# Optimization experiments

Hardware: AMD Instinct MI355X
Metric: run time of the kernel (lower is better)

The kernel has to match this reference:

```python
import jax, jax.numpy as jnp
import numpy as np

T, N, XD, H, Z, E = 6, 4096, 64, 256, 128, 131072


def setup_inputs() -> dict:
    key = jax.random.key(0)
    ks = jax.random.split(key, 16)
    f32 = jnp.float32
    def rn(k, shp):
        return jax.random.normal(k, shp, f32)
    def gl(k, shp):  # glorot-ish init, scaled by fan_in
        return jax.random.normal(k, shp, f32) * np.float32(1.0 / np.sqrt(shp[-2]))
    return {
        "x": rn(ks[0], (T, N, XD)),
        "edges": jax.random.randint(ks[1], (T, 2, E), 0, N, dtype=jnp.int32),
        "eps": rn(ks[2], (T, N, Z)),
        "drop_u": jax.random.uniform(ks[3], (T, N, Z), f32),
        "phi_x_w": gl(ks[4], (XD, H)), "phi_x_b": jnp.zeros((H,), f32),
        "phi_z_w": gl(ks[5], (Z, H)), "phi_z_b": jnp.zeros((H,), f32),
        "enc_w": gl(ks[6], (2 * H, H)),
        "enc_mu_w": gl(ks[7], (H, Z)),
        "enc_lv_w": gl(ks[8], (H, Z)),
        "prior_w": gl(ks[9], (H, H)), "prior_b": jnp.zeros((H,), f32),
        "prior_mu_w": gl(ks[10], (H, Z)), "prior_mu_b": jnp.zeros((Z,), f32),
        "prior_lv_w": gl(ks[11], (H, Z)), "prior_lv_b": jnp.zeros((Z,), f32),
        "gru_wx": gl(ks[12], (4, 2 * H, H)),  # gates i,f,o,c; x-side GCN weights
        "gru_wh": gl(ks[13], (4, H, H)),      # gates i,f,o,c; h-side GCN weights
    }


def reference(x, edges, eps, drop_u, phi_x_w, phi_x_b, phi_z_w, phi_z_b,
              enc_w, enc_mu_w, enc_lv_w, prior_w, prior_b,
              prior_mu_w, prior_mu_b, prior_lv_w, prior_lv_b,
              gru_wx, gru_wh):
    T_, N_, _ = x.shape
    H_ = phi_x_w.shape[1]
    h = jnp.zeros((N_, H_), x.dtype)
    c = jnp.zeros((N_, H_), x.dtype)
    loop = jnp.arange(N_, dtype=edges.dtype)
    enc_mus, prior_mus = [], []
    dec_t = None
    for t in range(T_):  # fixed small T; edge structure differs per step
        row = jnp.concatenate([edges[t, 0], loop])  # add self loops
        col = jnp.concatenate([edges[t, 1], loop])
        deg = jax.ops.segment_sum(jnp.ones(row.shape, x.dtype), row, num_segments=N_)
        dinv = jnp.where(deg > 0, jax.lax.rsqrt(deg), jnp.zeros((), x.dtype))
        norm = (dinv[row] * dinv[col])[:, None]

        def gcn(xx, W):
            # GCNConv: xW, gather at col, scale by sym-norm, scatter-add at row
            return jax.ops.segment_sum(norm * (xx @ W)[col], row, num_segments=N_)

        phi_x_t = jax.nn.relu(x[t] @ phi_x_w + phi_x_b)
        enc_t = jax.nn.relu(gcn(jnp.concatenate([phi_x_t, h], axis=1), enc_w))
        enc_mu_t = gcn(enc_t, enc_mu_w)
        enc_std_t = jax.nn.softplus(gcn(enc_t, enc_lv_w))
        prior_t = jax.nn.relu(h @ prior_w + prior_b)
        prior_mu_t = prior_t @ prior_mu_w + prior_mu_b
        _prior_std_t = jax.nn.softplus(prior_t @ prior_lv_w + prior_lv_b)  # computed as in original, unused in returns
        z_t = eps[t] * enc_std_t + enc_mu_t  # original: eps.mul(logvar).add_(mu)
        phi_z_t = jax.nn.relu(z_t @ phi_z_w + phi_z_b)
        # InnerProductDecoder with dropout(p=0.5, training=True), identity act
        z_drop = jnp.where(drop_u[t] < 0.5, z_t * 2.0, jnp.zeros((), x.dtype))
        dec_t = z_drop @ z_drop.T  # [N, N]
        # graph-LSTM step (n_layer = 1)
        xin = jnp.concatenate([phi_x_t, phi_z_t], axis=1)  # [N, 2H]
        gi = jax.nn.sigmoid(gcn(xin, gru_wx[0]) + gcn(h, gru_wh[0]))
        gf = jax.nn.sigmoid(gcn(xin, gru_wx[1]) + gcn(h, gru_wh[1]))
        go = jax.nn.sigmoid(gcn(xin, gru_wx[2]) + gcn(h, gru_wh[2]))
        ct = jnp.tanh(gcn(xin, gru_wx[3]) + gcn(h, gru_wh[3]))
        c_new = gf * h + gi * ct    # faithful to original: F_g * h[i] (not c)
        h_new = go * jnp.tanh(c)    # faithful to original: uses old c[i]
        h, c = h_new, c_new
        enc_mus.append(enc_mu_t)
        prior_mus.append(prior_mu_t)
    return jnp.stack(enc_mus), jnp.stack(prior_mus), h[None], dec_t
```

## Files before the change

### kernel.cpp

```cpp
#include <hip/hip_runtime.h>
#include <hip/hip_bf16.h>
#include <math.h>

#define T_  6
#define NN  4096
#define XD_ 64
#define H_  256
#define ZZ  128
#define EE  131072

typedef unsigned short u16;
typedef __attribute__((ext_vector_type(8))) short short8;
typedef __attribute__((ext_vector_type(4))) float f32x4;

__device__ __forceinline__ float bf2f(u16 u) { return __uint_as_float(((unsigned)u) << 16); }
__device__ __forceinline__ u16 f2bf(float f) {
    unsigned x = __float_as_uint(f);
    return (u16)((x + 0x7FFFu + ((x >> 16) & 1u)) >> 16);
}

__global__ void k_deg(const int* __restrict__ edges, int* __restrict__ degcnt) {
    int t = blockIdx.y;
    int e = blockIdx.x * 256 + threadIdx.x;
    const int* rows = edges + (size_t)t * 2 * EE;
    atomicAdd(&degcnt[t * NN + rows[e]], 1);
}

__global__ void k_scan_dinv(const int* __restrict__ degcnt_all,
                            int* __restrict__ row_start_all,
                            int* __restrict__ cursor_all,
                            float* __restrict__ dinv_all) {
    __shared__ int sbuf[1024];
    int tt = blockIdx.x;
    const int* degcnt = degcnt_all + tt * NN;
    int* row_start = row_start_all + tt * (NN + 1);
    int* cursor = cursor_all + tt * NN;
    float* dinv = dinv_all + tt * NN;
    int t = threadIdx.x;
    int b = t * 4;
    int v0 = degcnt[b + 0], v1 = degcnt[b + 1], v2 = degcnt[b + 2], v3 = degcnt[b + 3];
    dinv[b + 0] = rsqrtf((float)(v0 + 1));
    dinv[b + 1] = rsqrtf((float)(v1 + 1));
    dinv[b + 2] = rsqrtf((float)(v2 + 1));
    dinv[b + 3] = rsqrtf((float)(v3 + 1));
    int s = v0 + v1 + v2 + v3;
    sbuf[t] = s;
    __syncthreads();
    for (int off = 1; off < 1024; off <<= 1) {
        int x = sbuf[t];
        int y = (t >= off) ? sbuf[t - off] : 0;
        __syncthreads();
        sbuf[t] = x + y;
        __syncthreads();
    }
    int excl = sbuf[t] - s;
    int r0 = excl, r1 = excl + v0, r2 = r1 + v1, r3 = r2 + v2;
    row_start[b + 0] = r0; cursor[b + 0] = r0;
    row_start[b + 1] = r1; cursor[b + 1] = r1;
    row_start[b + 2] = r2; cursor[b + 2] = r2;
    row_start[b + 3] = r3; cursor[b + 3] = r3;
    if (t == 1023) row_start[NN] = r3 + v3;
}

__global__ void k_scatter(const int* __restrict__ edges,
                          int* __restrict__ cursor, const float* __restrict__ dinv,
                          int* __restrict__ col_idx, float* __restrict__ val) {
    int t = blockIdx.y;
    int e = blockIdx.x * 256 + threadIdx.x;
    const int* rows = edges + (size_t)t * 2 * EE;
    const int* cols = rows + EE;
    int r = rows[e], cc = cols[e];
    int pos = atomicAdd(&cursor[t * NN + r], 1);
    col_idx[(size_t)t * EE + pos] = cc;
    val[(size_t)t * EE + pos] = dinv[t * NN + r] * dinv[t * NN + cc];
}

__device__ __forceinline__ void sp_row(const u16* __restrict__ Y,
                                       const int* __restrict__ row_start,
                                       const int* __restrict__ col_idx,
                                       const float* __restrict__ val,
                                       const float* __restrict__ dinv,
                                       u16* __restrict__ outp, int ldo,
                                       int r, float (*red)[64][4]) {
    int lane = threadIdx.x & 63, w = threadIdx.x >> 6;
    int s0 = row_start[r], s1 = row_start[r + 1];
    int deg = s1 - s0;
    int e0 = s0 + ((deg * w) >> 2);
    int e1 = s0 + ((deg * (w + 1)) >> 2);
    float a1[4] = {0.f, 0.f, 0.f, 0.f};
    for (int base = e0; base < e1; base += 64) {
        int n = e1 - base; if (n > 64) n = 64;
        int cl = 0; float vl = 0.f;
        if (base + lane < e1) { cl = col_idx[base + lane]; vl = val[base + lane]; }
        for (int e = 0; e < n; ++e) {
            int cc = __shfl(cl, e);
            float v = __shfl(vl, e);
            ushort4 y = *(const ushort4*)(Y + (size_t)cc * H_ + lane * 4);
            a1[0] += v * bf2f(y.x); a1[1] += v * bf2f(y.y);
            a1[2] += v * bf2f(y.z); a1[3] += v * bf2f(y.w);
        }
    }
#pragma unroll
    for (int j = 0; j < 4; ++j) red[w][lane][j] = a1[j];
    __syncthreads();
    if (w == 0) {
        float dr = dinv[r], sc = dr * dr;
#pragma unroll
        for (int j = 0; j < 4; ++j)
#pragma unroll
            for (int ww = 1; ww < 4; ++ww) a1[j] += red[ww][lane][j];
        ushort4 ys = *(const ushort4*)(Y + (size_t)r * H_ + lane * 4);
        a1[0] += sc * bf2f(ys.x); a1[1] += sc * bf2f(ys.y);
        a1[2] += sc * bf2f(ys.z); a1[3] += sc * bf2f(ys.w);
        *(ushort4*)(outp + (size_t)r * ldo + lane * 4) =
            make_ushort4(f2bf(a1[0]), f2bf(a1[1]), f2bf(a1[2]), f2bf(a1[3]));
    }
}

__global__ void k_spmm(const u16* __restrict__ Y1,
                       const int* __restrict__ row_start_all, const int* __restrict__ col_idx_all,
                       const float* __restrict__ val_all, const float* __restrict__ dinv_all,
                       u16* __restrict__ out1, int ldo,
                       long long sY, long long sO) {
    __shared__ float red[4][64][4];
    int t = blockIdx.y;
    sp_row(Y1 + (size_t)t * sY, row_start_all + (size_t)t * (NN + 1),
           col_idx_all + (size_t)t * EE, val_all + (size_t)t * EE,
           dinv_all + (size_t)t * NN, out1 + (size_t)t * sO, ldo,
           blockIdx.x, red);
}

template<int MF>
__device__ __forceinline__ void mm_core(const u16* __restrict__ A, int lda,
                                        const u16* __restrict__ BT, int ldbt, int K,
                                        int row0, int col0,
                                        f32x4 acc[MF][MF], char* smem) {
    constexpr int TILE = MF * 32;
    u16* As = (u16*)smem;
    u16* Bs = As + TILE * 64;
    const int lane = threadIdx.x & 63;
    const int w = threadIdx.x >> 6;
    const int wr = (w >> 1) * (TILE / 2);
    const int wc = (w & 1) * (TILE / 2);

    int gRow[MF], gCol[MF];
#pragma unroll
    for (int i = 0; i < MF; ++i) {
        int G = (w * MF + i) * 64 + lane;
        int r = G >> 3;
        gRow[i] = r;
        gCol[i] = ((G & 7) ^ (r & 7)) << 3;
    }

    for (int k0 = 0; k0 < K; k0 += 64) {
#pragma unroll
        for (int i = 0; i < MF; ++i) {
            const u16* sa = A + (size_t)(row0 + gRow[i]) * lda + k0 + gCol[i];
            __builtin_amdgcn_global_load_lds(
                (const __attribute__((address_space(1))) void*)sa,
                (__attribute__((address_space(3))) void*)(As + (w * MF + i) * 512), 16, 0, 0);
            const u16* sb = BT + (size_t)(col0 + gRow[i]) * ldbt + k0 + gCol[i];
            __builtin_amdgcn_global_load_lds(
                (const __attribute__((address_space(1))) void*)sb,
                (__attribute__((address_space(3))) void*)(Bs + (w * MF + i) * 512), 16, 0, 0);
        }
        __syncthreads();
#pragma unroll
        for (int kk = 0; kk < 2; ++kk) {
            short8 a[MF], b[MF];
#pragma unroll
            for (int mf = 0; mf < MF; ++mf) {
                int r = wr + mf * 16 + (lane & 15);
                int off = (r * 128 + kk * 64 + (lane >> 4) * 16) ^ ((r & 7) << 4);
                a[mf] = *(const short8*)((const char*)As + off);
            }
#pragma unroll
            for (int nf = 0; nf < MF; ++nf) {
                int r = wc + nf * 16 + (lane & 15);
                int off = (r * 128 + kk * 64 + (lane >> 4) * 16) ^ ((r & 7) << 4);
                b[nf] = *(const short8*)((const char*)Bs + off);
            }
#pragma unroll
            for (int mf = 0; mf < MF; ++mf)
#pragma unroll
                for (int nf = 0; nf < MF; ++nf)
                    acc[mf][nf] = __builtin_amdgcn_mfma_f32_16x16x32_bf16(
                        a[mf], b[nf], acc[mf][nf], 0, 0, 0);
        }
        __syncthreads();
    }
}

template<int MF>
__launch_bounds__(256)
__global__ void k_mm(const u16* __restrict__ A, int lda,
                     const u16* __restrict__ BT, int ldbt, int K,
                     float* __restrict__ C0, int ldc0,
                     u16* __restrict__ C1, int ldc1,
                     const float* __restrict__ bias, int act,
                     float* __restrict__ C2,
                     const float* __restrict__ du, u16* __restrict__ zdOut) {
    constexpr int TILE = MF * 32;
    constexpr int STAGE_B = TILE * 64 * 2 * 2;
    constexpr int EPI_B = (MF == 2) ? 64 * 68 * 4 : 0;
    constexpr int SMEM_B = STAGE_B > EPI_B ? STAGE_B : EPI_B;
    __shared__ alignas(16) char smem[SMEM_B];

    const int tid = threadIdx.x;
    const int lane = tid & 63;
    const int w = tid >> 6;
    const int row0 = blockIdx.y * TILE;
    const int col0 = blockIdx.x * TILE;
    const int wr = (w >> 1) * (TILE / 2);
    const int wc = (w & 1) * (TILE / 2);

    f32x4 acc[MF][MF];
#pragma unroll
    for (int i = 0; i < MF; ++i)
#pragma unroll
        for (int j = 0; j < MF; ++j)
            acc[i][j] = f32x4{0.f, 0.f, 0.f, 0.f};

    mm_core<MF>(A, lda, BT, ldbt, K, row0, col0, acc, smem);

    const int ci = lane & 15;
    const int ri = (lane >> 4) * 4;

    if constexpr (MF == 2) {
        if (act == 4) {
            float (*epi)[68] = (float(*)[68])smem;
#pragma unroll
            for (int mf = 0; mf < 2; ++mf)
#pragma unroll
                for (int nf = 0; nf < 2; ++nf)
#pragma unroll
                    for (int i = 0; i < 4; ++i)
                        epi[wr + mf * 16 + ri + i][wc + nf * 16 + ci] = acc[mf][nf][i];
            __syncthreads();
            float* muo = C0; const float* eps = C2; u16* zo = C1;
#pragma unroll
            for (int k = 0; k < 8; ++k) {
                int p = tid + k * 256;
                int row = p >> 5, jl = p & 31;
                float mu = epi[row][jl * 2];
                float sp = epi[row][jl * 2 + 1];
                float sd = (sp > 20.f) ? sp : log1pf(expf(sp));
                int idx = (row0 + row) * ZZ + (col0 >> 1) + jl;
                muo[idx] = mu;
                u16 z16 = f2bf(eps[idx] * sd + mu);
                zo[idx] = z16;
                if (zdOut)
                    zdOut[idx] = (du[idx] < 0.5f) ? f2bf(2.f * bf2f(z16)) : (u16)0;
            }
            return;
        }
    }

#pragma unroll
    for (int mf = 0; mf < MF; ++mf) {
#pragma unroll
        for (int nf = 0; nf < MF; ++nf) {
            int row = row0 + wr + mf * 16 + ri;
            int col = col0 + wc + nf * 16 + ci;
            if (C1) {
                float bv = bias ? bias[col] : 0.f;
#pragma unroll
                for (int i = 0; i < 4; ++i) {
                    float v = acc[mf][nf][i] + bv;
                    if (act == 1) v = fmaxf(v, 0.f);
                    C1[(size_t)(row + i) * ldc1 + col] = f2bf(v);
                }
            } else {
                float bv = bias ? bias[col] : 0.f;
#pragma unroll
                for (int i = 0; i < 4; ++i)
                    C0[(size_t)(row + i) * ldc0 + col] = acc[mf][nf][i] + bv;
            }
        }
    }
}

__launch_bounds__(256)
__global__ void k_dual(const u16* __restrict__ A0, int lda0, const u16* __restrict__ BT0,
                       int ldbt0, int K0, u16* __restrict__ C0d, int ldc0d,
                       const float* __restrict__ b0,
                       const u16* __restrict__ A1, int lda1, const u16* __restrict__ BT1,
                       int ldbt1, int K1, u16* __restrict__ C1d, int ldc1d,
                       const float* __restrict__ b1) {
    __shared__ alignas(16) char smem[16384];
    const int z = blockIdx.z;
    const u16* A = z ? A1 : A0;   int lda = z ? lda1 : lda0;
    const u16* BT = z ? BT1 : BT0; int ldbt = z ? ldbt1 : ldbt0;
    int K = z ? K1 : K0;
    u16* C = z ? C1d : C0d;       int ldc = z ? ldc1d : ldc0d;
    const float* bias = z ? b1 : b0;

    const int lane = threadIdx.x & 63;
    const int w = threadIdx.x >> 6;
    const int row0 = blockIdx.y * 64;
    const int col0 = blockIdx.x * 64;
    const int wr = (w >> 1) * 32, wc = (w & 1) * 32;

    f32x4 acc[2][2];
#pragma unroll
    for (int i = 0; i < 2; ++i)
#pragma unroll
        for (int j = 0; j < 2; ++j) acc[i][j] = f32x4{0.f, 0.f, 0.f, 0.f};
    mm_core<2>(A, lda, BT, ldbt, K, row0, col0, acc, smem);

    const int ci = lane & 15, ri = (lane >> 4) * 4;
#pragma unroll
    for (int mf = 0; mf < 2; ++mf)
#pragma unroll
        for (int nf = 0; nf < 2; ++nf) {
            int row = row0 + wr + mf * 16 + ri;
            int col = col0 + wc + nf * 16 + ci;
            float bv = bias ? bias[col] : 0.f;
#pragma unroll
            for (int i = 0; i < 4; ++i)
                C[(size_t)(row + i) * ldc + col] = f2bf(fmaxf(acc[mf][nf][i] + bv, 0.f));
        }
}

__launch_bounds__(256)
__global__ void k_sp_mm(const u16* __restrict__ Y, const int* __restrict__ row_start,
                        const int* __restrict__ col_idx, const float* __restrict__ val,
                        const float* __restrict__ dinv, u16* __restrict__ spOut,
                        const u16* __restrict__ A, int lda, const u16* __restrict__ BT,
                        int ldbt, int K, float* __restrict__ C0, int ldc0,
                        const float* __restrict__ bias) {
    __shared__ alignas(16) char smem[16384];
    int bid = blockIdx.x;
    if (bid < NN) {
        sp_row(Y, row_start, col_idx, val, dinv, spOut, H_, bid, (float(*)[64][4])smem);
        return;
    }
    int b2 = bid - NN;
    const int row0 = (b2 >> 1) * 64;
    const int col0 = (b2 & 1) * 64;
    const int lane = threadIdx.x & 63;
    const int w = threadIdx.x >> 6;
    const int wr = (w >> 1) * 32, wc = (w & 1) * 32;
    f32x4 acc[2][2];
#pragma unroll
    for (int i = 0; i < 2; ++i)
#pragma unroll
        for (int j = 0; j < 2; ++j) acc[i][j] = f32x4{0.f, 0.f, 0.f, 0.f};
    mm_core<2>(A, lda, BT, ldbt, K, row0, col0, acc, smem);
    const int ci = lane & 15, ri = (lane >> 4) * 4;
#pragma unroll
    for (int mf = 0; mf < 2; ++mf)
#pragma unroll
        for (int nf = 0; nf < 2; ++nf) {
            int row = row0 + wr + mf * 16 + ri;
            int col = col0 + wc + nf * 16 + ci;
            float bv = bias[col];
#pragma unroll
            for (int i = 0; i < 4; ++i)
                C0[(size_t)(row + i) * ldc0 + col] = acc[mf][nf][i] + bv;
        }
}

__launch_bounds__(256)
__global__ void k_gates(const u16* __restrict__ XIN, const u16* __restrict__ BgT,
                        float* __restrict__ h, float* __restrict__ c,
                        u16* __restrict__ hbf, float* __restrict__ hOut,
                        int skipSH) {
    __shared__ alignas(16) char smem[64 * 68 * 4];
    u16* As = (u16*)smem;
    u16* Bs = As + 64 * 64;
    const int tid = threadIdx.x;
    const int lane = tid & 63;
    const int w = tid >> 6;
    const int row0 = blockIdx.y * 64;
    const int col0 = blockIdx.x * 64;
    const int wr = (w >> 1) * 32;
    const int wc = (w & 1) * 32;

    f32x4 acc[2][2];
#pragma unroll
    for (int i = 0; i < 2; ++i)
#pragma unroll
        for (int j = 0; j < 2; ++j) acc[i][j] = f32x4{0.f, 0.f, 0.f, 0.f};

    int gRow[2], gCol[2];
#pragma unroll
    for (int i = 0; i < 2; ++i) {
        int G = (w * 2 + i) * 64 + lane;
        int r = G >> 3;
        gRow[i] = r;
        gCol[i] = ((G & 7) ^ (r & 7)) << 3;
    }

    const int nIter = skipSH ? 8 : 12;
    for (int it = 0; it < nIter; ++it) {
        int k0 = it * 64 + ((skipSH && it >= 4) ? 256 : 0);
#pragma unroll
        for (int i = 0; i < 2; ++i) {
            const u16* sa = XIN + (size_t)(row0 + gRow[i]) * 768 + k0 + gCol[i];
            __builtin_amdgcn_global_load_lds(
                (const __attribute__((address_space(1))) void*)sa,
                (__attribute__((address_space(3))) void*)(As + (w * 2 + i) * 512), 16, 0, 0);
            const u16* sb = BgT + (size_t)(col0 + gRow[i]) * 768 + k0 + gCol[i];
            __builtin_amdgcn_global_load_lds(
                (const __attribute__((address_space(1))) void*)sb,
                (__attribute__((address_space(3))) void*)(Bs + (w * 2 + i) * 512), 16, 0, 0);
        }
        __syncthreads();
#pragma unroll
        for (int kk = 0; kk < 2; ++kk) {
            short8 a[2], b[2];
#pragma unroll
            for (int mf = 0; mf < 2; ++mf) {
                int r = wr + mf * 16 + (lane & 15);
                int off = (r * 128 + kk * 64 + (lane >> 4) * 16) ^ ((r & 7) << 4);
                a[mf] = *(const short8*)((const char*)As + off);
            }
#pragma unroll
            for (int nf = 0; nf < 2; ++nf) {
                int r = wc + nf * 16 + (lane & 15);
                int off = (r * 128 + kk * 64 + (lane >> 4) * 16) ^ ((r & 7) << 4);
                b[nf] = *(const short8*)((const char*)Bs + off);
            }
#pragma unroll
            for (int mf = 0; mf < 2; ++mf)
#pragma unroll
                for (int nf = 0; nf < 2; ++nf)
                    acc[mf][nf] = __builtin_amdgcn_mfma_f32_16x16x32_bf16(
                        a[mf], b[nf], acc[mf][nf], 0, 0, 0);
        }
        __syncthreads();
    }

    const int ci = lane & 15;
    const int ri = (lane >> 4) * 4;
    float (*epi)[68] = (float(*)[68])smem;
#pragma unroll
    for (int mf = 0; mf < 2; ++mf)
#pragma unroll
        for (int nf = 0; nf < 2; ++nf)
#pragma unroll
            for (int i = 0; i < 4; ++i)
                epi[wr + mf * 16 + ri + i][wc + nf * 16 + ci] = acc[mf][nf][i];
    __syncthreads();
#pragma unroll
    for (int k = 0; k < 4; ++k) {
        int p = tid + k * 256;
        int row = p >> 4, jl = p & 15;
        float4 g4 = *(const float4*)&epi[row][jl * 4];
        float gi = 1.f / (1.f + expf(-g4.x));
        float gf = 1.f / (1.f + expf(-g4.y));
        float go = 1.f / (1.f + expf(-g4.z));
        float ct = tanhf(g4.w);
        int idx = (row0 + row) * H_ + (col0 >> 2) + jl;
        float ho = h[idx], co = c[idx];
        float cn = gf * ho + gi * ct;
        float hn = go * tanhf(co);
        h[idx] = hn;
        c[idx] = cn;
        hbf[idx] = f2bf(hn);
        if (hOut) hOut[idx] = hn;
    }
}

__global__ void k_cvt(const float* __restrict__ in, u16* __restrict__ outp, int n4) {
    int i = blockIdx.x * 256 + threadIdx.x;
    if (i >= n4) return;
    float4 v = ((const float4*)in)[i];
    ((ushort4*)outp)[i] = make_ushort4(f2bf(v.x), f2bf(v.y), f2bf(v.z), f2bf(v.w));
}

__global__ void k_prep(const float* __restrict__ phi_x_w, const float* __restrict__ phi_z_w,
                       const float* __restrict__ enc_w, const float* __restrict__ prior_w,
                       const float* __restrict__ prior_mu_w,
                       const float* __restrict__ enc_mu_w, const float* __restrict__ enc_lv_w,
                       const float* __restrict__ gru_wx, const float* __restrict__ gru_wh,
                       u16* __restrict__ phi_x_wT, u16* __restrict__ phi_z_wT,
                       u16* __restrict__ enc_wT, u16* __restrict__ prior_wT,
                       u16* __restrict__ prior_mu_wT, u16* __restrict__ mulvT,
                       u16* __restrict__ BgT) {
    int idx = blockIdx.x * 256 + threadIdx.x;
    if (idx < 16384) {
        int j = idx >> 6, k = idx & 63;
        phi_x_wT[idx] = f2bf(phi_x_w[k * 256 + j]);
        return;
    }
    idx -= 16384;
    if (idx < 32768) {
        int j = idx >> 7, k = idx & 127;
        phi_z_wT[idx] = f2bf(phi_z_w[k * 256 + j]);
        return;
    }
    idx -= 32768;
    if (idx < 131072) {
        int j = idx >> 9, k = idx & 511;
        enc_wT[idx] = f2bf(enc_w[k * 256 + j]);
        return;
    }
    idx -= 131072;
    if (idx < 65536) {
        int j = idx >> 8, k = idx & 255;
        prior_wT[idx] = f2bf(prior_w[k * 256 + j]);
        return;
    }
    idx -= 65536;
    if (idx < 32768) {
        int j = idx >> 8, k = idx & 255;
        prior_mu_wT[idx] = f2bf(prior_mu_w[k * 128 + j]);
        return;
    }
    idx -= 32768;
    if (idx < 65536) {
        int cp = idx >> 8, k = idx & 255;
        int j = cp >> 1, s = cp & 1;
        float v = s ? enc_lv_w[k * 128 + j] : enc_mu_w[k * 128 + j];
        mulvT[idx] = f2bf(v);
        return;
    }
    idx -= 65536;
    if (idx < 786432) {
        int cp = idx / 768, k = idx % 768;
        int g = cp & 3, j = cp >> 2;
        float v;
        if (k < 256)      v = gru_wx[((size_t)g * 512 + k) * 256 + j];
        else if (k < 512) v = gru_wh[((size_t)g * 256 + (k - 256)) * 256 + j];
        else              v = gru_wx[((size_t)g * 512 + (k - 256)) * 256 + j];
        BgT[idx] = f2bf(v);
    }
}

extern "C" void kernel_launch(void* const* d_in, const int* in_sizes, int n_in,
                              void* d_out_v, int out_size, void* d_ws, size_t ws_size,
                              hipStream_t stream) {
    (void)in_sizes; (void)n_in; (void)out_size;
    const float* x          = (const float*)d_in[0];
    const int*   edges      = (const int*)d_in[1];
    const float* eps        = (const float*)d_in[2];
    const float* drop_u     = (const float*)d_in[3];
    const float* phi_x_w    = (const float*)d_in[4];
    const float* phi_x_b    = (const float*)d_in[5];
    const float* phi_z_w    = (const float*)d_in[6];
    const float* phi_z_b    = (const float*)d_in[7];
    const float* enc_w      = (const float*)d_in[8];
    const float* enc_mu_w   = (const float*)d_in[9];
    const float* enc_lv_w   = (const float*)d_in[10];
    const float* prior_w    = (const float*)d_in[11];
    const float* prior_b    = (const float*)d_in[12];
    const float* prior_mu_w = (const float*)d_in[13];
    const float* prior_mu_b = (const float*)d_in[14];
    const float* gru_wx     = (const float*)d_in[17];
    const float* gru_wh     = (const float*)d_in[18];
    float* out = (float*)d_out_v;

    char* base = (char*)d_ws;
    size_t cur = 0;
    auto carve = [&](size_t bytes) -> void* {
        void* p = base + cur;
        cur += (bytes + 255) & ~(size_t)255;
        return p;
    };
    float* h         = (float*)carve((size_t)NN * H_ * 4);
    float* c         = (float*)carve((size_t)NN * H_ * 4);
    u16* h_bf        = (u16*)carve((size_t)NN * H_ * 2);
    size_t hcz_bytes = cur;
    float* dinv      = (float*)carve((size_t)T_ * NN * 4);
    int*   degcnt    = (int*)carve((size_t)T_ * NN * 4);
    int*   row_start = (int*)carve((size_t)T_ * (NN + 1) * 4);
    int*   cursor    = (int*)carve((size_t)T_ * NN * 4);
    int*   col_idx   = (int*)carve((size_t)T_ * EE * 4);
    float* val       = (float*)carve((size_t)T_ * EE * 4);
    u16* x_bf        = (u16*)carve((size_t)T_ * NN * XD_ * 2);
    u16* phi6        = (u16*)carve((size_t)T_ * NN * H_ * 2);
    u16* phi         = (u16*)carve((size_t)NN * H_ * 2);
    u16* enc_t       = (u16*)carve((size_t)NN * H_ * 2);
    u16* SEb         = (u16*)carve((size_t)NN * H_ * 2);
    u16* prior_t     = (u16*)carve((size_t)NN * H_ * 2);
    u16* XIN6        = (u16*)carve((size_t)T_ * NN * 768 * 2);
    u16* zbuf        = (u16*)carve((size_t)NN * ZZ * 2);
    u16* zd          = (u16*)carve((size_t)NN * ZZ * 2);
    u16* phi_x_wT    = (u16*)carve((size_t)XD_ * H_ * 2);
    u16* phi_z_wT    = (u16*)carve((size_t)ZZ * H_ * 2);
    u16* enc_wT      = (u16*)carve((size_t)512 * H_ * 2);
    u16* prior_wT    = (u16*)carve((size_t)H_ * H_ * 2);
    u16* prior_mu_wT = (u16*)carve((size_t)ZZ * H_ * 2);
    u16* mulvT       = (u16*)carve((size_t)H_ * H_ * 2);
    u16* BgT         = (u16*)carve((size_t)1024 * 768 * 2);
    if (cur > ws_size) return;

    const size_t NZ = (size_t)NN * ZZ;
    const size_t HOFF = (size_t)2 * T_ * NZ;
    const size_t DECOFF = HOFF + (size_t)NN * H_;

    k_cvt<<<(T_ * NN * XD_ / 4 + 255) / 256, 256, 0, stream>>>(x, x_bf, T_ * NN * XD_ / 4);
    k_prep<<<(1130496 + 255) / 256, 256, 0, stream>>>(
        phi_x_w, phi_z_w, enc_w, prior_w, prior_mu_w, enc_mu_w, enc_lv_w,
        gru_wx, gru_wh,
        phi_x_wT, phi_z_wT, enc_wT, prior_wT, prior_mu_wT, mulvT, BgT);

    hipMemsetAsync(degcnt, 0, (size_t)T_ * NN * 4, stream);
    k_deg<<<dim3(EE / 256, T_), 256, 0, stream>>>(edges, degcnt);
    k_scan_dinv<<<T_, 1024, 0, stream>>>(degcnt, row_start, cursor, dinv);
    k_scatter<<<dim3(EE / 256, T_), 256, 0, stream>>>(edges, cursor, dinv, col_idx, val);

    k_mm<2><<<dim3(4, (T_ * NN) / 64), 256, 0, stream>>>(x_bf, XD_, phi_x_wT, XD_, XD_,
        nullptr, 0, phi6, H_, phi_x_b, 1, nullptr, nullptr, nullptr);
    k_spmm<<<dim3(NN, T_), 256, 0, stream>>>(phi6, row_start, col_idx, val, dinv,
        XIN6, 768, (long long)NN * H_, (long long)NN * 768);

    hipMemsetAsync(h, 0, hcz_bytes, stream);

    for (int t = 0; t < T_; ++t) {
        const int* rs_t = row_start + (size_t)t * (NN + 1);
        const int* ci_t = col_idx + (size_t)t * EE;
        const float* vv_t = val + (size_t)t * EE;
        const float* dv_t = dinv + (size_t)t * NN;
        u16* xin_t = XIN6 + (size_t)t * NN * 768;
        int last = (t == T_ - 1);

        if (t > 0)
            k_spmm<<<dim3(NN, 1), 256, 0, stream>>>(h_bf, rs_t, ci_t, vv_t, dv_t,
                                                    xin_t + 256, 768, 0, 0);
        k_dual<<<dim3(4, 64, 2), 256, 0, stream>>>(
            xin_t, 768, enc_wT, 512, (t == 0) ? 256 : 512, enc_t, H_, nullptr,
            h_bf, H_, prior_wT, H_, H_, prior_t, H_, prior_b);
        k_sp_mm<<<NN + 128, 256, 0, stream>>>(enc_t, rs_t, ci_t, vv_t, dv_t, SEb,
            prior_t, H_, prior_mu_wT, H_, H_,
            out + (size_t)(T_ + t) * NZ, ZZ, prior_mu_b);
        k_mm<2><<<dim3(4, 64), 256, 0, stream>>>(SEb, H_, mulvT, H_, H_,
            out + (size_t)t * NZ, 0, zbuf, 0, nullptr, 4, (float*)(eps + (size_t)t * NZ),
            last ? drop_u + (size_t)t * NZ : nullptr, last ? zd : nullptr);
        k_mm<2><<<dim3(4, 64), 256, 0, stream>>>(zbuf, ZZ, phi_z_wT, ZZ, ZZ,
            nullptr, 0, phi, H_, phi_z_b, 1, nullptr, nullptr, nullptr);
        k_spmm<<<dim3(NN, 1), 256, 0, stream>>>(phi, rs_t, ci_t, vv_t, dv_t,
                                                xin_t + 512, 768, 0, 0);
        k_gates<<<dim3(16, 64), 256, 0, stream>>>(xin_t, BgT, h, c, h_bf,
            last ? out + HOFF : nullptr, t == 0);
    }

    k_mm<4><<<dim3(32, 32), 256, 0, stream>>>(zd, ZZ, zd, ZZ, ZZ,
        out + DECOFF, NN, nullptr, 0, nullptr, 0, nullptr, nullptr, nullptr);
}
```

Baseline: 613.6 us.

## Use one wave per SpMM row, regroup kernel fusions, enlarge gate tile

The sparse row aggregation now gives each wavefront a whole row, with two edges in flight per iteration and 16-byte loads. This removes the LDS reduction and __syncthreads across four waves, and each block now covers four rows. The per-step kernel pairing is reshuffled: the h-side SpMM is fused with the prior matmul, and the prior-mu matmul is fused into k_dual, whose z-slice skips its unused column blocks. The enc SpMM becomes a standalone launch. k_gates uses 128-row tiles, so fewer blocks each reuse the weight tile across more rows, at the cost of more registers and LDS per block.

```diff
diff --git a/kernel.cpp b/kernel.cpp
--- a/kernel.cpp
+++ b/kernel.cpp
@@ -11,6 +11,7 @@
 
 typedef unsigned short u16;
 typedef __attribute__((ext_vector_type(8))) short short8;
+typedef __attribute__((ext_vector_type(8))) unsigned short u16x8;
 typedef __attribute__((ext_vector_type(4))) float f32x4;
 
 __device__ __forceinline__ float bf2f(u16 u) { return __uint_as_float(((unsigned)u) << 16); }
@@ -75,45 +76,39 @@
     val[(size_t)t * EE + pos] = dinv[t * NN + r] * dinv[t * NN + cc];
 }
 
-__device__ __forceinline__ void sp_row(const u16* __restrict__ Y,
-                                       const int* __restrict__ row_start,
-                                       const int* __restrict__ col_idx,
-                                       const float* __restrict__ val,
-                                       const float* __restrict__ dinv,
-                                       u16* __restrict__ outp, int ldo,
-                                       int r, float (*red)[64][4]) {
-    int lane = threadIdx.x & 63, w = threadIdx.x >> 6;
+__device__ __forceinline__ void sp_row_wave(const u16* __restrict__ Y,
+                                            const int* __restrict__ row_start,
+                                            const int* __restrict__ col_idx,
+                                            const float* __restrict__ val,
+                                            const float* __restrict__ dinv,
+                                            u16* __restrict__ outp, int ldo, int r) {
+    int lane = threadIdx.x & 63;
+    int half = lane >> 5;
+    int cg = lane & 31;
     int s0 = row_start[r], s1 = row_start[r + 1];
-    int deg = s1 - s0;
-    int e0 = s0 + ((deg * w) >> 2);
-    int e1 = s0 + ((deg * (w + 1)) >> 2);
-    float a1[4] = {0.f, 0.f, 0.f, 0.f};
-    for (int base = e0; base < e1; base += 64) {
-        int n = e1 - base; if (n > 64) n = 64;
+    float a[8] = {0.f, 0.f, 0.f, 0.f, 0.f, 0.f, 0.f, 0.f};
+    for (int base = s0; base < s1; base += 64) {
+        int n = s1 - base; if (n > 64) n = 64;
         int cl = 0; float vl = 0.f;
-        if (base + lane < e1) { cl = col_idx[base + lane]; vl = val[base + lane]; }
-        for (int e = 0; e < n; ++e) {
-            int cc = __shfl(cl, e);
-            float v = __shfl(vl, e);
-            ushort4 y = *(const ushort4*)(Y + (size_t)cc * H_ + lane * 4);
-            a1[0] += v * bf2f(y.x); a1[1] += v * bf2f(y.y);
-            a1[2] += v * bf2f(y.z); a1[3] += v * bf2f(y.w);
-        }
-    }
-#pragma unroll
-    for (int j = 0; j < 4; ++j) red[w][lane][j] = a1[j];
-    __syncthreads();
-    if (w == 0) {
+        if (base + lane < s1) { cl = col_idx[base + lane]; vl = val[base + lane]; }
+        for (int e = 0; e < n; e += 2) {
+            int ei = e + half;
+            int cc = __shfl(cl, ei);
+            float v = (ei < n) ? __shfl(vl, ei) : 0.f;
+            u16x8 y = *(const u16x8*)(Y + (size_t)cc * H_ + cg * 8);
+#pragma unroll
+            for (int j = 0; j < 8; ++j) a[j] += v * bf2f(y[j]);
+        }
+    }
+#pragma unroll
+    for (int j = 0; j < 8; ++j) a[j] += __shfl_xor(a[j], 32);
+    if (half == 0) {
         float dr = dinv[r], sc = dr * dr;
-#pragma unroll
-        for (int j = 0; j < 4; ++j)
-#pragma unroll
-            for (int ww = 1; ww < 4; ++ww) a1[j] += red[ww][lane][j];
-        ushort4 ys = *(const ushort4*)(Y + (size_t)r * H_ + lane * 4);
-        a1[0] += sc * bf2f(ys.x); a1[1] += sc * bf2f(ys.y);
-        a1[2] += sc * bf2f(ys.z); a1[3] += sc * bf2f(ys.w);
-        *(ushort4*)(outp + (size_t)r * ldo + lane * 4) =
-            make_ushort4(f2bf(a1[0]), f2bf(a1[1]), f2bf(a1[2]), f2bf(a1[3]));
+        u16x8 ys = *(const u16x8*)(Y + (size_t)r * H_ + cg * 8);
+        u16x8 o;
+#pragma unroll
+        for (int j = 0; j < 8; ++j) o[j] = f2bf(a[j] + sc * bf2f(ys[j]));
+        *(u16x8*)(outp + (size_t)r * ldo + cg * 8) = o;
     }
 }
 
@@ -122,12 +117,12 @@
                        const float* __restrict__ val_all, const float* __restrict__ dinv_all,
                        u16* __restrict__ out1, int ldo,
                        long long sY, long long sO) {
-    __shared__ float red[4][64][4];
     int t = blockIdx.y;
-    sp_row(Y1 + (size_t)t * sY, row_start_all + (size_t)t * (NN + 1),
-           col_idx_all + (size_t)t * EE, val_all + (size_t)t * EE,
-           dinv_all + (size_t)t * NN, out1 + (size_t)t * sO, ldo,
-           blockIdx.x, red);
+    int w = threadIdx.x >> 6;
+    sp_row_wave(Y1 + (size_t)t * sY, row_start_all + (size_t)t * (NN + 1),
+                col_idx_all + (size_t)t * EE, val_all + (size_t)t * EE,
+                dinv_all + (size_t)t * NN, out1 + (size_t)t * sO, ldo,
+                blockIdx.x * 4 + w);
 }
 
 template<int MF>
@@ -282,18 +277,16 @@
 
 __launch_bounds__(256)
 __global__ void k_dual(const u16* __restrict__ A0, int lda0, const u16* __restrict__ BT0,
-                       int ldbt0, int K0, u16* __restrict__ C0d, int ldc0d,
-                       const float* __restrict__ b0,
+                       int ldbt0, int K0, u16* __restrict__ Cb0, int ldcb0,
                        const u16* __restrict__ A1, int lda1, const u16* __restrict__ BT1,
-                       int ldbt1, int K1, u16* __restrict__ C1d, int ldc1d,
-                       const float* __restrict__ b1) {
+                       int ldbt1, int K1, float* __restrict__ Cf1, int ldcf1,
+                       const float* __restrict__ bias1) {
     __shared__ alignas(16) char smem[16384];
     const int z = blockIdx.z;
+    if (z && blockIdx.x >= 2) return;
     const u16* A = z ? A1 : A0;   int lda = z ? lda1 : lda0;
     const u16* BT = z ? BT1 : BT0; int ldbt = z ? ldbt1 : ldbt0;
     int K = z ? K1 : K0;
-    u16* C = z ? C1d : C0d;       int ldc = z ? ldc1d : ldc0d;
-    const float* bias = z ? b1 : b0;
 
     const int lane = threadIdx.x & 63;
     const int w = threadIdx.x >> 6;
@@ -315,29 +308,39 @@
         for (int nf = 0; nf < 2; ++nf) {
             int row = row0 + wr + mf * 16 + ri;
             int col = col0 + wc + nf * 16 + ci;
-            float bv = bias ? bias[col] : 0.f;
-#pragma unroll
-            for (int i = 0; i < 4; ++i)
-                C[(size_t)(row + i) * ldc + col] = f2bf(fmaxf(acc[mf][nf][i] + bv, 0.f));
+            if (z == 0) {
+#pragma unroll
+                for (int i = 0; i < 4; ++i)
+                    Cb0[(size_t)(row + i) * ldcb0 + col] = f2bf(fmaxf(acc[mf][nf][i], 0.f));
+            } else {
+                float bv = bias1[col];
+#pragma unroll
+                for (int i = 0; i < 4; ++i)
+                    Cf1[(size_t)(row + i) * ldcf1 + col] = acc[mf][nf][i] + bv;
+            }
         }
 }
 
 __launch_bounds__(256)
 __global__ void k_sp_mm(const u16* __restrict__ Y, const int* __restrict__ row_start,
                         const int* __restrict__ col_idx, const float* __restrict__ val,
-                        const float* __restrict__ dinv, u16* __restrict__ spOut,
+                        const float* __restrict__ dinv, u16* __restrict__ spOut, int spLdo,
+                        int doSp,
                         const u16* __restrict__ A, int lda, const u16* __restrict__ BT,
-                        int ldbt, int K, float* __restrict__ C0, int ldc0,
-                        const float* __restrict__ bias) {
+                        int ldbt, int K, float* __restrict__ Cf, int ldcf,
+                        u16* __restrict__ Cb, int ldcb,
+                        const float* __restrict__ bias, int gx) {
     __shared__ alignas(16) char smem[16384];
     int bid = blockIdx.x;
-    if (bid < NN) {
-        sp_row(Y, row_start, col_idx, val, dinv, spOut, H_, bid, (float(*)[64][4])smem);
+    if (bid < NN / 4) {
+        if (!doSp) return;
+        int w = threadIdx.x >> 6;
+        sp_row_wave(Y, row_start, col_idx, val, dinv, spOut, spLdo, bid * 4 + w);
         return;
     }
-    int b2 = bid - NN;
-    const int row0 = (b2 >> 1) * 64;
-    const int col0 = (b2 & 1) * 64;
+    int b2 = bid - NN / 4;
+    const int row0 = (b2 / gx) * 64;
+    const int col0 = (b2 % gx) * 64;
     const int lane = threadIdx.x & 63;
     const int w = threadIdx.x >> 6;
     const int wr = (w >> 1) * 32, wc = (w & 1) * 32;
@@ -354,10 +357,16 @@
         for (int nf = 0; nf < 2; ++nf) {
             int row = row0 + wr + mf * 16 + ri;
             int col = col0 + wc + nf * 16 + ci;
-            float bv = bias[col];
-#pragma unroll
-            for (int i = 0; i < 4; ++i)
-                C0[(size_t)(row + i) * ldc0 + col] = acc[mf][nf][i] + bv;
+            float bv = bias ? bias[col] : 0.f;
+            if (Cb) {
+#pragma unroll
+                for (int i = 0; i < 4; ++i)
+                    Cb[(size_t)(row + i) * ldcb + col] = f2bf(fmaxf(acc[mf][nf][i] + bv, 0.f));
+            } else {
+#pragma unroll
+                for (int i = 0; i < 4; ++i)
+                    Cf[(size_t)(row + i) * ldcf + col] = acc[mf][nf][i] + bv;
+            }
         }
 }
 
@@ -366,42 +375,53 @@
                         float* __restrict__ h, float* __restrict__ c,
                         u16* __restrict__ hbf, float* __restrict__ hOut,
                         int skipSH) {
-    __shared__ alignas(16) char smem[64 * 68 * 4];
+    __shared__ alignas(16) char smem[128 * 68 * 4];
     u16* As = (u16*)smem;
-    u16* Bs = As + 64 * 64;
+    u16* Bs = As + 128 * 64;
     const int tid = threadIdx.x;
     const int lane = tid & 63;
     const int w = tid >> 6;
-    const int row0 = blockIdx.y * 64;
+    const int row0 = blockIdx.y * 128;
     const int col0 = blockIdx.x * 64;
-    const int wr = (w >> 1) * 32;
+    const int wrB = (w >> 1) * 64;
     const int wc = (w & 1) * 32;
 
-    f32x4 acc[2][2];
-#pragma unroll
-    for (int i = 0; i < 2; ++i)
+    f32x4 acc[4][2];
+#pragma unroll
+    for (int i = 0; i < 4; ++i)
 #pragma unroll
         for (int j = 0; j < 2; ++j) acc[i][j] = f32x4{0.f, 0.f, 0.f, 0.f};
 
-    int gRow[2], gCol[2];
+    int aRow[4], aCol[4];
+#pragma unroll
+    for (int i = 0; i < 4; ++i) {
+        int G = (w * 4 + i) * 64 + lane;
+        int r = G >> 3;
+        aRow[i] = r;
+        aCol[i] = ((G & 7) ^ (r & 7)) << 3;
+    }
+    int bRow[2], bCol[2];
 #pragma unroll
     for (int i = 0; i < 2; ++i) {
         int G = (w * 2 + i) * 64 + lane;
         int r = G >> 3;
-        gRow[i] = r;
-        gCol[i] = ((G & 7) ^ (r & 7)) << 3;
+        bRow[i] = r;
+        bCol[i] = ((G & 7) ^ (r & 7)) << 3;
     }
 
     const int nIter = skipSH ? 8 : 12;
     for (int it = 0; it < nIter; ++it) {
         int k0 = it * 64 + ((skipSH && it >= 4) ? 256 : 0);
 #pragma unroll
-        for (int i = 0; i < 2; ++i) {
-            const u16* sa = XIN + (size_t)(row0 + gRow[i]) * 768 + k0 + gCol[i];
+        for (int i = 0; i < 4; ++i) {
+            const u16* sa = XIN + (size_t)(row0 + aRow[i]) * 768 + k0 + aCol[i];
             __builtin_amdgcn_global_load_lds(
                 (const __attribute__((address_space(1))) void*)sa,
-                (__attribute__((address_space(3))) void*)(As + (w * 2 + i) * 512), 16, 0, 0);
-            const u16* sb = BgT + (size_t)(col0 + gRow[i]) * 768 + k0 + gCol[i];
+                (__attribute__((address_space(3))) void*)(As + (w * 4 + i) * 512), 16, 0, 0);
+        }
+#pragma unroll
+        for (int i = 0; i < 2; ++i) {
+            const u16* sb = BgT + (size_t)(col0 + bRow[i]) * 768 + k0 + bCol[i];
             __builtin_amdgcn_global_load_lds(
                 (const __attribute__((address_space(1))) void*)sb,
                 (__attribute__((address_space(3))) void*)(Bs + (w * 2 + i) * 512), 16, 0, 0);
@@ -409,10 +429,10 @@
         __syncthreads();
 #pragma unroll
         for (int kk = 0; kk < 2; ++kk) {
-            short8 a[2], b[2];
-#pragma unroll
-            for (int mf = 0; mf < 2; ++mf) {
-                int r = wr + mf * 16 + (lane & 15);
+            short8 a[4], b[2];
+#pragma unroll
+            for (int mf = 0; mf < 4; ++mf) {
+                int r = wrB + mf * 16 + (lane & 15);
                 int off = (r * 128 + kk * 64 + (lane >> 4) * 16) ^ ((r & 7) << 4);
                 a[mf] = *(const short8*)((const char*)As + off);
             }
@@ -423,7 +443,7 @@
                 b[nf] = *(const short8*)((const char*)Bs + off);
             }
 #pragma unroll
-            for (int mf = 0; mf < 2; ++mf)
+            for (int mf = 0; mf < 4; ++mf)
 #pragma unroll
                 for (int nf = 0; nf < 2; ++nf)
                     acc[mf][nf] = __builtin_amdgcn_mfma_f32_16x16x32_bf16(
@@ -436,15 +456,15 @@
     const int ri = (lane >> 4) * 4;
     float (*epi)[68] = (float(*)[68])smem;
 #pragma unroll
-    for (int mf = 0; mf < 2; ++mf)
+    for (int mf = 0; mf < 4; ++mf)
 #pragma unroll
         for (int nf = 0; nf < 2; ++nf)
 #pragma unroll
             for (int i = 0; i < 4; ++i)
-                epi[wr + mf * 16 + ri + i][wc + nf * 16 + ci] = acc[mf][nf][i];
+                epi[wrB + mf * 16 + ri + i][wc + nf * 16 + ci] = acc[mf][nf][i];
     __syncthreads();
 #pragma unroll
-    for (int k = 0; k < 4; ++k) {
+    for (int k = 0; k < 8; ++k) {
         int p = tid + k * 256;
         int row = p >> 4, jl = p & 15;
         float4 g4 = *(const float4*)&epi[row][jl * 4];
@@ -604,7 +624,7 @@
 
     k_mm<2><<<dim3(4, (T_ * NN) / 64), 256, 0, stream>>>(x_bf, XD_, phi_x_wT, XD_, XD_,
         nullptr, 0, phi6, H_, phi_x_b, 1, nullptr, nullptr, nullptr);
-    k_spmm<<<dim3(NN, T_), 256, 0, stream>>>(phi6, row_start, col_idx, val, dinv,
+    k_spmm<<<dim3(NN / 4, T_), 256, 0, stream>>>(phi6, row_start, col_idx, val, dinv,
         XIN6, 768, (long long)NN * H_, (long long)NN * 768);
 
     hipMemsetAsync(h, 0, hcz_bytes, stream);
@@ -617,23 +637,23 @@
         u16* xin_t = XIN6 + (size_t)t * NN * 768;
         int last = (t == T_ - 1);
 
-        if (t > 0)
-            k_spmm<<<dim3(NN, 1), 256, 0, stream>>>(h_bf, rs_t, ci_t, vv_t, dv_t,
-                                                    xin_t + 256, 768, 0, 0);
+        k_sp_mm<<<NN / 4 + 256, 256, 0, stream>>>(h_bf, rs_t, ci_t, vv_t, dv_t,
+            xin_t + 256, 768, t > 0,
+            h_bf, H_, prior_wT, H_, H_, nullptr, 0, prior_t, H_, prior_b, 4);
         k_dual<<<dim3(4, 64, 2), 256, 0, stream>>>(
-            xin_t, 768, enc_wT, 512, (t == 0) ? 256 : 512, enc_t, H_, nullptr,
-            h_bf, H_, prior_wT, H_, H_, prior_t, H_, prior_b);
-        k_sp_mm<<<NN + 128, 256, 0, stream>>>(enc_t, rs_t, ci_t, vv_t, dv_t, SEb,
+            xin_t, 768, enc_wT, 512, (t == 0) ? 256 : 512, enc_t, H_,
             prior_t, H_, prior_mu_wT, H_, H_,
             out + (size_t)(T_ + t) * NZ, ZZ, prior_mu_b);
+        k_spmm<<<dim3(NN / 4, 1), 256, 0, stream>>>(enc_t, rs_t, ci_t, vv_t, dv_t,
+                                                    SEb, H_, 0, 0);
         k_mm<2><<<dim3(4, 64), 256, 0, stream>>>(SEb, H_, mulvT, H_, H_,
             out + (size_t)t * NZ, 0, zbuf, 0, nullptr, 4, (float*)(eps + (size_t)t * NZ),
             last ? drop_u + (size_t)t * NZ : nullptr, last ? zd : nullptr);
         k_mm<2><<<dim3(4, 64), 256, 0, stream>>>(zbuf, ZZ, phi_z_wT, ZZ, ZZ,
             nullptr, 0, phi, H_, phi_z_b, 1, nullptr, nullptr, nullptr);
-        k_spmm<<<dim3(NN, 1), 256, 0, stream>>>(phi, rs_t, ci_t, vv_t, dv_t,
-                                                xin_t + 512, 768, 0, 0);
-        k_gates<<<dim3(16, 64), 256, 0, stream>>>(xin_t, BgT, h, c, h_bf,
+        k_spmm<<<dim3(NN / 4, 1), 256, 0, stream>>>(phi, rs_t, ci_t, vv_t, dv_t,
+                                                    xin_t + 512, 768, 0, 0);
+        k_gates<<<dim3(16, 32), 256, 0, stream>>>(xin_t, BgT, h, c, h_bf,
             last ? out + HOFF : nullptr, t == 0);
     }
 
```

New measurement: 611.1 us. No clear change (-0.4%).
